# Performance work log

Measured on AMD Instinct MI355X. Metric: run time of the kernel, lower is better.

Reference implementation:

```python
import jax, jax.numpy as jnp
import numpy as np

EPS = 1e-10
B, S, D, K = 8, 2048, 512, 1024
TEMP = 1.0  # quantizer temperature set to 1.0 in SQVAE.__init__


def _ln(x, g, b):
    m = x.mean(-1, keepdims=True)
    v = x.var(-1, keepdims=True)
    return (x - m) / jnp.sqrt(v + 1e-5) * g + b


def _mlp(x, w1, b1, g1, be1, w2, b2, g2, be2):
    # feed_forward: Linear -> ReLU -> LayerNorm, twice (MLPLayers=2)
    h = _ln(jax.nn.relu(x @ w1 + b1), g1, be1)
    return _ln(jax.nn.relu(h @ w2 + b2), g2, be2)


def setup_inputs() -> dict:
    key = jax.random.key(0)
    ks = jax.random.split(key, 20)
    W = 0.04  # small init scale to keep distances / softmax well-conditioned
    p = lambda k, sh, s=1.0: jax.random.normal(k, sh, dtype=jnp.float32) * s
    return {
        'x': p(ks[0], (B, S, D)),
        'gumbel_u': jax.random.uniform(ks[1], (B * S, K), dtype=jnp.float32),
        'enc_w1': p(ks[2], (D, D), W), 'enc_b1': jnp.zeros(D, jnp.float32),
        'enc_g1': jnp.ones(D, jnp.float32), 'enc_be1': jnp.zeros(D, jnp.float32),
        'enc_w2': p(ks[3], (D, D), W), 'enc_b2': jnp.zeros(D, jnp.float32),
        'enc_g2': jnp.ones(D, jnp.float32), 'enc_be2': jnp.zeros(D, jnp.float32),
        'dec_w1': p(ks[4], (D, D), W), 'dec_b1': jnp.zeros(D, jnp.float32),
        'dec_g1': jnp.ones(D, jnp.float32), 'dec_be1': jnp.zeros(D, jnp.float32),
        'dec_w2': p(ks[5], (D, D), W), 'dec_b2': jnp.zeros(D, jnp.float32),
        'dec_g2': jnp.ones(D, jnp.float32), 'dec_be2': jnp.zeros(D, jnp.float32),
        'codebook': p(ks[6], (K, D)),
        'log_param_q': jnp.zeros((), jnp.float32),
    }


def reference(x, gumbel_u, enc_w1, enc_b1, enc_g1, enc_be1, enc_w2, enc_b2, enc_g2, enc_be2,
              dec_w1, dec_b1, dec_g1, dec_be1, dec_w2, dec_b2, dec_g2, dec_be2,
              codebook, log_param_q):
    bs, seq, d = x.shape
    z = _mlp(x, enc_w1, enc_b1, enc_g1, enc_be1, enc_w2, enc_b2, enc_g2, enc_be2)
    # gaussian_1: log_var_q = 0 -> var_q = exp(log_param_q_scalar)
    var_q = jnp.exp(log_param_q)
    w = 0.5 / jnp.clip(var_q, 1e-10)  # 0.5 * precision_q (scalar)
    zf = z.reshape(-1, d)  # [N, D]
    # cdist^2 style distance, scaled by weight -> logits [N, K]
    dist = w * (jnp.sum(zf * zf, axis=1, keepdims=True)
                + jnp.sum(codebook * codebook, axis=1)
                - 2.0 * zf @ codebook.T)
    logit = -dist
    logp = jax.nn.log_softmax(logit, axis=-1)
    probs = jnp.exp(logp)
    # gumbel-softmax sample (train path), noise provided as uniform input
    g = -jnp.log(-jnp.log(gumbel_u + EPS) + EPS)
    encodings = jax.nn.softmax((logit + g) / TEMP, axis=-1)
    z_q = (encodings @ codebook).reshape(bs, seq, d)
    kld_discrete = jnp.sum(probs * logp) / bs
    kld_continuous = jnp.mean(jnp.sum((z - z_q) ** 2 * w, axis=(1, 2)))
    loss = kld_discrete + kld_continuous
    avg_probs = jnp.mean(jax.lax.stop_gradient(probs), axis=0)
    perplexity = jnp.exp(-jnp.sum(avg_probs * jnp.log(avg_probs + 1e-7)))
    x_rec = _mlp(z_q, dec_w1, dec_b1, dec_g1, dec_be1, dec_w2, dec_b2, dec_g2, dec_be2)
    return x_rec, loss, perplexity
```

## Files before the change

### kernel.cpp

```cpp
#include <hip/hip_runtime.h>
#include <math.h>

#define NROWS 16384
#define DIM   512
#define KCODE 1024

typedef __attribute__((ext_vector_type(8))) __bf16 bf16x8;
typedef __attribute__((ext_vector_type(4))) float f32x4;

__device__ __forceinline__ float wave_reduce_sum(float v) {
  #pragma unroll
  for (int m = 1; m < 64; m <<= 1) v += __shfl_xor(v, m, 64);
  return v;
}
__device__ __forceinline__ float wave_reduce_max(float v) {
  #pragma unroll
  for (int m = 1; m < 64; m <<= 1) v = fmaxf(v, __shfl_xor(v, m, 64));
  return v;
}
__device__ __forceinline__ unsigned short f2bf(float f) {
  union { float f; unsigned u; } v; v.f = f;
  unsigned r = v.u + 0x7FFFu + ((v.u >> 16) & 1u);
  return (unsigned short)(r >> 16);
}
__device__ __forceinline__ float bf2f(unsigned short h) {
  union { unsigned u; float f; } v; v.u = ((unsigned)h) << 16;
  return v.f;
}
__device__ __forceinline__ uint4 pack8(const float* x) {
  uint4 r;
  r.x = (unsigned)f2bf(x[0]) | ((unsigned)f2bf(x[1]) << 16);
  r.y = (unsigned)f2bf(x[2]) | ((unsigned)f2bf(x[3]) << 16);
  r.z = (unsigned)f2bf(x[4]) | ((unsigned)f2bf(x[5]) << 16);
  r.w = (unsigned)f2bf(x[6]) | ((unsigned)f2bf(x[7]) << 16);
  return r;
}

__device__ __forceinline__ void glds16(const void* g, void* lds) {
  __builtin_amdgcn_global_load_lds(
      (const __attribute__((address_space(1))) unsigned int*)g,
      (__attribute__((address_space(3))) unsigned int*)lds, 16, 0, 0);
}

template <int NPASS, int EPI, int K, int N, int LDA>
__global__ __launch_bounds__(256) void gemm_bt(
    const unsigned short* A0, const unsigned short* A1, const unsigned short* A2,
    const unsigned short* B0, const unsigned short* B1, const unsigned short* B2,
    const float* __restrict__ bias,
    const float* __restrict__ znorm, const float* __restrict__ cnorm,
    const float* __restrict__ lpq,
    const unsigned short* __restrict__ zh, const unsigned short* __restrict__ zl,
    float* __restrict__ kldc,
    unsigned short* __restrict__ outb, float* __restrict__ outf) {
  __shared__ char smem[32768];
  const int t = threadIdx.x;
  const int l = t & 63, w = t >> 6;
  const int wm = w >> 1, wn = w & 1;
  const int NTN = N / 128;
  const int b = blockIdx.x;
  const int xcd = b & 7;
  const int j = b >> 3;
  const int m0 = (xcd * 16 + j / NTN) * 128;
  const int n0 = (j % NTN) * 128;

  f32x4 acc[4][4];
  #pragma unroll
  for (int i = 0; i < 4; ++i)
    #pragma unroll
    for (int jj = 0; jj < 4; ++jj) acc[i][jj] = (f32x4){0.f, 0.f, 0.f, 0.f};

  const int row_lo = w * 16 + (l & 15);
  const int row_hi = (w + 4) * 16 + (l & 15);
  const int kcol = (l >> 4) * 8;
  const int dA0 = w * 1024;
  const int dA1 = (w + 4) * 1024;
  const int dB0 = 8192 + w * 1024;
  const int dB1 = 8192 + (w + 4) * 1024;

  const unsigned short* APs[3] = {A0, A1, A2};
  const unsigned short* BPs[3] = {B0, B1, B2};

  #pragma unroll 1
  for (int p = 0; p < NPASS; ++p) {
    const unsigned short* aA0 = APs[p] + (size_t)(m0 + row_lo) * LDA + kcol;
    const unsigned short* aA1 = APs[p] + (size_t)(m0 + row_hi) * LDA + kcol;
    const unsigned short* aB0 = BPs[p] + (size_t)(n0 + row_lo) * K + kcol;
    const unsigned short* aB1 = BPs[p] + (size_t)(n0 + row_hi) * K + kcol;
    glds16(aA0, smem + dA0);
    glds16(aA1, smem + dA1);
    glds16(aB0, smem + dB0);
    glds16(aB1, smem + dB1);
    __syncthreads();
    #pragma unroll 1
    for (int kt = 0; kt < K; kt += 32) {
      const int cur = (kt >> 5) & 1;
      const int nxt = cur ^ 1;
      if (kt + 32 < K) {
        char* nb = smem + nxt * 16384;
        glds16(aA0 + kt + 32, nb + dA0);
        glds16(aA1 + kt + 32, nb + dA1);
        glds16(aB0 + kt + 32, nb + dB0);
        glds16(aB1 + kt + 32, nb + dB1);
      }
      const unsigned short* Ab = (const unsigned short*)(smem + cur * 16384);
      const unsigned short* Bb = (const unsigned short*)(smem + cur * 16384 + 8192);
      bf16x8 af[4], bfr[4];
      #pragma unroll
      for (int i = 0; i < 4; ++i) {
        af[i]  = *(const bf16x8*)&Ab[((wm * 4 + i) * 64 + l) * 8];
        bfr[i] = *(const bf16x8*)&Bb[((wn * 4 + i) * 64 + l) * 8];
      }
      #pragma unroll
      for (int mi = 0; mi < 4; ++mi)
        #pragma unroll
        for (int ni = 0; ni < 4; ++ni)
          acc[mi][ni] = __builtin_amdgcn_mfma_f32_16x16x32_bf16(af[mi], bfr[ni], acc[mi][ni], 0, 0, 0);
      __syncthreads();
    }
  }

  float* slab = (float*)(smem + w * 4352);
  const int q = l >> 4, c16 = l & 15;
  const int rr = l >> 4, c4 = (l & 15) * 4;
  const float wq = (EPI >= 1) ? 0.5f / fmaxf(expf(lpq[0]), 1e-10f) : 0.f;
  float local = 0.f;

  #pragma unroll
  for (int mi = 0; mi < 4; ++mi) {
    __syncthreads();
    #pragma unroll
    for (int ni = 0; ni < 4; ++ni)
      #pragma unroll
      for (int r = 0; r < 4; ++r)
        slab[(q * 4 + r) * 68 + ni * 16 + c16] = acc[mi][ni][r];
    __syncthreads();
    #pragma unroll
    for (int pp = 0; pp < 4; ++pp) {
      const int row = pp * 4 + rr;
      const float4 v4 = *(const float4*)&slab[row * 68 + c4];
      float v[4] = {v4.x, v4.y, v4.z, v4.w};
      const int m = m0 + wm * 64 + mi * 16 + row;
      const int nc = n0 + wn * 64 + c4;
      if (EPI == 0) {
        const float4 b4 = *(const float4*)&bias[nc];
        v[0] = fmaxf(v[0] + b4.x, 0.f);
        v[1] = fmaxf(v[1] + b4.y, 0.f);
        v[2] = fmaxf(v[2] + b4.z, 0.f);
        v[3] = fmaxf(v[3] + b4.w, 0.f);
        uint2 st;
        st.x = (unsigned)f2bf(v[0]) | ((unsigned)f2bf(v[1]) << 16);
        st.y = (unsigned)f2bf(v[2]) | ((unsigned)f2bf(v[3]) << 16);
        *(uint2*)&outb[(size_t)m * N + nc] = st;
      } else if (EPI == 1) {
        const float zn = znorm[m];
        const float4 cn = *(const float4*)&cnorm[nc];
        float4 o;
        o.x = -wq * (zn + cn.x - 2.f * v[0]);
        o.y = -wq * (zn + cn.y - 2.f * v[1]);
        o.z = -wq * (zn + cn.z - 2.f * v[2]);
        o.w = -wq * (zn + cn.w - 2.f * v[3]);
        *(float4*)&outf[(size_t)m * N + nc] = o;
      } else {
        const uint2 h2 = *(const uint2*)&zh[(size_t)m * N + nc];
        const uint2 l2 = *(const uint2*)&zl[(size_t)m * N + nc];
        const float z0 = bf2f((unsigned short)(h2.x & 0xFFFF)) + bf2f((unsigned short)(l2.x & 0xFFFF));
        const float z1 = bf2f((unsigned short)(h2.x >> 16))    + bf2f((unsigned short)(l2.x >> 16));
        const float z2 = bf2f((unsigned short)(h2.y & 0xFFFF)) + bf2f((unsigned short)(l2.y & 0xFFFF));
        const float z3 = bf2f((unsigned short)(h2.y >> 16))    + bf2f((unsigned short)(l2.y >> 16));
        const float d0 = z0 - v[0], d1 = z1 - v[1], d2 = z2 - v[2], d3 = z3 - v[3];
        local += d0 * d0 + d1 * d1 + d2 * d2 + d3 * d3;
        uint2 st;
        st.x = (unsigned)f2bf(v[0]) | ((unsigned)f2bf(v[1]) << 16);
        st.y = (unsigned)f2bf(v[2]) | ((unsigned)f2bf(v[3]) << 16);
        *(uint2*)&outb[(size_t)m * N + nc] = st;
      }
    }
  }
  if (EPI == 2) {
    local = wave_reduce_sum(local) * wq;
    if (l == 0) atomicAdd(kldc, local);
  }
}

template <int MODE>
__global__ __launch_bounds__(256) void ln_rows(
    const unsigned short* __restrict__ X, const float* __restrict__ g,
    const float* __restrict__ be, unsigned short* __restrict__ Y,
    unsigned short* __restrict__ Yl, float* __restrict__ znorm,
    float* __restrict__ Yf) {
  const int l = threadIdx.x & 63, wv = threadIdx.x >> 6;
  float gv[8], bv[8];
  {
    const float4 a = *(const float4*)&g[l * 8];
    const float4 b = *(const float4*)&g[l * 8 + 4];
    gv[0] = a.x; gv[1] = a.y; gv[2] = a.z; gv[3] = a.w;
    gv[4] = b.x; gv[5] = b.y; gv[6] = b.z; gv[7] = b.w;
    const float4 c = *(const float4*)&be[l * 8];
    const float4 d = *(const float4*)&be[l * 8 + 4];
    bv[0] = c.x; bv[1] = c.y; bv[2] = c.z; bv[3] = c.w;
    bv[4] = d.x; bv[5] = d.y; bv[6] = d.z; bv[7] = d.w;
  }
  const int row0 = blockIdx.x * 32 + wv * 8;
  for (int rr = 0; rr < 8; ++rr) {
    const int row = row0 + rr;
    const uint4 raw = *(const uint4*)&X[(size_t)row * 512 + l * 8];
    float v[8];
    const unsigned rw[4] = {raw.x, raw.y, raw.z, raw.w};
    #pragma unroll
    for (int i = 0; i < 4; ++i) {
      v[2 * i]     = bf2f((unsigned short)(rw[i] & 0xFFFF));
      v[2 * i + 1] = bf2f((unsigned short)(rw[i] >> 16));
    }
    float s = 0.f, ss = 0.f;
    #pragma unroll
    for (int i = 0; i < 8; ++i) { s += v[i]; ss += v[i] * v[i]; }
    #pragma unroll
    for (int m = 1; m < 64; m <<= 1) {
      s += __shfl_xor(s, m, 64);
      ss += __shfl_xor(ss, m, 64);
    }
    const float mean = s * (1.f / 512.f);
    const float var = ss * (1.f / 512.f) - mean * mean;
    const float rstd = rsqrtf(var + 1e-5f);
    float y[8];
    #pragma unroll
    for (int i = 0; i < 8; ++i) y[i] = (v[i] - mean) * rstd * gv[i] + bv[i];
    if (MODE == 0) {
      *(uint4*)&Y[(size_t)row * 512 + l * 8] = pack8(y);
    } else if (MODE == 1) {
      float lo[8], ns = 0.f;
      unsigned short hx[8];
      #pragma unroll
      for (int i = 0; i < 8; ++i) {
        hx[i] = f2bf(y[i]);
        lo[i] = y[i] - bf2f(hx[i]);
        ns += y[i] * y[i];
      }
      uint4 hv;
      hv.x = (unsigned)hx[0] | ((unsigned)hx[1] << 16);
      hv.y = (unsigned)hx[2] | ((unsigned)hx[3] << 16);
      hv.z = (unsigned)hx[4] | ((unsigned)hx[5] << 16);
      hv.w = (unsigned)hx[6] | ((unsigned)hx[7] << 16);
      *(uint4*)&Y[(size_t)row * 512 + l * 8] = hv;
      *(uint4*)&Yl[(size_t)row * 512 + l * 8] = pack8(lo);
      ns = wave_reduce_sum(ns);
      if (l == 0) znorm[row] = ns;
    } else {
      float4 o0, o1;
      o0.x = y[0]; o0.y = y[1]; o0.z = y[2]; o0.w = y[3];
      o1.x = y[4]; o1.y = y[5]; o1.z = y[6]; o1.w = y[7];
      *(float4*)&Yf[(size_t)row * 512 + l * 8] = o0;
      *(float4*)&Yf[(size_t)row * 512 + l * 8 + 4] = o1;
    }
  }
}

__global__ __launch_bounds__(256) void convert_f32_bf16(
    const float* __restrict__ X, unsigned short* __restrict__ Y) {
  const size_t i = ((size_t)blockIdx.x * 256 + threadIdx.x) * 8;
  const float4 a = *(const float4*)&X[i];
  const float4 b = *(const float4*)&X[i + 4];
  float v[8] = {a.x, a.y, a.z, a.w, b.x, b.y, b.z, b.w};
  *(uint4*)&Y[i] = pack8(v);
}

__global__ __launch_bounds__(256) void prep_cb(
    const float* __restrict__ CB, unsigned short* __restrict__ H,
    unsigned short* __restrict__ L, float* __restrict__ cnorm) {
  const int wv = threadIdx.x >> 6, l = threadIdx.x & 63;
  const int r = blockIdx.x * 4 + wv;
  const float* row = &CB[(size_t)r * 512 + l * 8];
  const float4 a = *(const float4*)row;
  const float4 b = *(const float4*)(row + 4);
  float x[8] = {a.x, a.y, a.z, a.w, b.x, b.y, b.z, b.w};
  float s = 0.f, lo[8];
  unsigned short hi[8];
  #pragma unroll
  for (int i = 0; i < 8; ++i) {
    s += x[i] * x[i];
    hi[i] = f2bf(x[i]);
    lo[i] = x[i] - bf2f(hi[i]);
  }
  uint4 hv;
  hv.x = (unsigned)hi[0] | ((unsigned)hi[1] << 16);
  hv.y = (unsigned)hi[2] | ((unsigned)hi[3] << 16);
  hv.z = (unsigned)hi[4] | ((unsigned)hi[5] << 16);
  hv.w = (unsigned)hi[6] | ((unsigned)hi[7] << 16);
  *(uint4*)&H[(size_t)r * 512 + l * 8] = hv;
  *(uint4*)&L[(size_t)r * 512 + l * 8] = pack8(lo);
  s = wave_reduce_sum(s);
  if (l == 0) cnorm[r] = s;
}

__global__ __launch_bounds__(256) void transpose_f32_bf16(
    const float* __restrict__ in, unsigned short* __restrict__ out, int R, int C) {
  __shared__ float tile[32][33];
  const int ntc = C >> 5;
  const int c0 = (blockIdx.x % ntc) * 32, r0 = (blockIdx.x / ntc) * 32;
  const int tx = threadIdx.x & 31, ty = threadIdx.x >> 5;
  #pragma unroll
  for (int i = 0; i < 4; ++i)
    tile[ty + 8 * i][tx] = in[(size_t)(r0 + ty + 8 * i) * C + c0 + tx];
  __syncthreads();
  #pragma unroll
  for (int i = 0; i < 4; ++i)
    out[(size_t)(c0 + ty + 8 * i) * R + r0 + tx] = f2bf(tile[tx][ty + 8 * i]);
}

__global__ __launch_bounds__(256) void softmax_gumbel(
    const float* logits, const float* __restrict__ U, unsigned short* E,
    float* __restrict__ colsum, float* __restrict__ kldd_acc) {
  __shared__ float cs[1024];
  __shared__ float kd[4];
  const int t = threadIdx.x;
  const int wv = t >> 6, l = t & 63;
  #pragma unroll
  for (int i = 0; i < 4; ++i) cs[t + 256 * i] = 0.f;
  __syncthreads();
  float psum[16];
  #pragma unroll
  for (int i = 0; i < 16; ++i) psum[i] = 0.f;
  float kldd = 0.f;
  const int nbase = blockIdx.x * 16 + wv * 4;

  for (int it = 0; it < 4; ++it) {
    const int row = nbase + it;
    const size_t off = (size_t)row * KCODE + 4 * l;
    float v[16];
    #pragma unroll
    for (int jj = 0; jj < 4; ++jj) {
      const float4 t4 = *(const float4*)&logits[off + 256 * jj];
      v[4 * jj + 0] = t4.x; v[4 * jj + 1] = t4.y; v[4 * jj + 2] = t4.z; v[4 * jj + 3] = t4.w;
    }
    float m = v[0];
    #pragma unroll
    for (int i = 1; i < 16; ++i) m = fmaxf(m, v[i]);
    m = wave_reduce_max(m);
    float se = 0.f;
    #pragma unroll
    for (int i = 0; i < 16; ++i) se += expf(v[i] - m);
    se = wave_reduce_sum(se);
    const float lz = logf(se);
    float pl = 0.f;
    #pragma unroll
    for (int i = 0; i < 16; ++i) {
      const float lp = v[i] - m - lz;
      const float p = expf(lp);
      psum[i] += p;
      pl += p * lp;
    }
    kldd += pl;
    float y[16];
    #pragma unroll
    for (int jj = 0; jj < 4; ++jj) {
      const float4 t4 = *(const float4*)&U[off + 256 * jj];
      y[4 * jj + 0] = v[4 * jj + 0] - logf(-logf(t4.x + 1e-10f) + 1e-10f);
      y[4 * jj + 1] = v[4 * jj + 1] - logf(-logf(t4.y + 1e-10f) + 1e-10f);
      y[4 * jj + 2] = v[4 * jj + 2] - logf(-logf(t4.z + 1e-10f) + 1e-10f);
      y[4 * jj + 3] = v[4 * jj + 3] - logf(-logf(t4.w + 1e-10f) + 1e-10f);
    }
    float m2 = y[0];
    #pragma unroll
    for (int i = 1; i < 16; ++i) m2 = fmaxf(m2, y[i]);
    m2 = wave_reduce_max(m2);
    float s2 = 0.f;
    #pragma unroll
    for (int i = 0; i < 16; ++i) s2 += expf(y[i] - m2);
    s2 = wave_reduce_sum(s2);
    const float inv = 1.f / s2;
    #pragma unroll
    for (int jj = 0; jj < 4; ++jj) {
      ushort4 e;
      e.x = f2bf(expf(y[4 * jj + 0] - m2) * inv);
      e.y = f2bf(expf(y[4 * jj + 1] - m2) * inv);
      e.z = f2bf(expf(y[4 * jj + 2] - m2) * inv);
      e.w = f2bf(expf(y[4 * jj + 3] - m2) * inv);
      *(ushort4*)&E[(size_t)row * 2048 + 4 * l + 256 * jj] = e;
    }
  }
  #pragma unroll
  for (int jj = 0; jj < 4; ++jj)
    #pragma unroll
    for (int c = 0; c < 4; ++c)
      atomicAdd(&cs[256 * jj + 4 * l + c], psum[4 * jj + c]);
  kldd = wave_reduce_sum(kldd);
  if (l == 0) kd[wv] = kldd;
  __syncthreads();
  #pragma unroll
  for (int i = 0; i < 4; ++i) {
    const float vv = cs[t + 256 * i];
    if (vv != 0.f) atomicAdd(&colsum[t + 256 * i], vv);
  }
  if (t == 0) atomicAdd(kldd_acc, kd[0] + kd[1] + kd[2] + kd[3]);
}

__global__ __launch_bounds__(256) void finalize(
    const float* __restrict__ colsum, const float* __restrict__ scal,
    float* __restrict__ out) {
  const int t = threadIdx.x;
  float ent = 0.f;
  #pragma unroll
  for (int jj = 0; jj < 4; ++jj) {
    const float a = colsum[t + 256 * jj] * (1.f / 16384.f);
    ent += a * logf(a + 1e-7f);
  }
  ent = wave_reduce_sum(ent);
  __shared__ float red[4];
  if ((t & 63) == 0) red[t >> 6] = ent;
  __syncthreads();
  if (t == 0) {
    const float tot = red[0] + red[1] + red[2] + red[3];
    out[0] = (scal[0] + scal[1]) * (1.f / 8.f);
    out[1] = expf(-tot);
  }
}

extern "C" void kernel_launch(void* const* d_in, const int* in_sizes, int n_in,
                              void* d_out, int out_size, void* d_ws, size_t ws_size,
                              hipStream_t stream) {
  const float* x      = (const float*)d_in[0];
  const float* gu     = (const float*)d_in[1];
  const float* enc_w1 = (const float*)d_in[2];
  const float* enc_b1 = (const float*)d_in[3];
  const float* enc_g1 = (const float*)d_in[4];
  const float* enc_e1 = (const float*)d_in[5];
  const float* enc_w2 = (const float*)d_in[6];
  const float* enc_b2 = (const float*)d_in[7];
  const float* enc_g2 = (const float*)d_in[8];
  const float* enc_e2 = (const float*)d_in[9];
  const float* dec_w1 = (const float*)d_in[10];
  const float* dec_b1 = (const float*)d_in[11];
  const float* dec_g1 = (const float*)d_in[12];
  const float* dec_e1 = (const float*)d_in[13];
  const float* dec_w2 = (const float*)d_in[14];
  const float* dec_b2 = (const float*)d_in[15];
  const float* dec_g2 = (const float*)d_in[16];
  const float* dec_e2 = (const float*)d_in[17];
  const float* cb     = (const float*)d_in[18];
  const float* lpq    = (const float*)d_in[19];
  float* out = (float*)d_out;
  char* wsb = (char*)d_ws;

  float*          logits = (float*)(wsb + 0);
  unsigned short* Eb     = (unsigned short*)(wsb + 0);
  unsigned short* t1     = (unsigned short*)(wsb + 67108864);
  unsigned short* xb     = (unsigned short*)(wsb + 83886080);
  unsigned short* zh     = xb;
  unsigned short* hq     = (unsigned short*)(wsb + 100663296);
  unsigned short* zl     = (unsigned short*)(wsb + 117440512);
  unsigned short* wt0    = (unsigned short*)(wsb + 134217728);
  unsigned short* wt1    = wt0 + 262144;
  unsigned short* wt2    = wt1 + 262144;
  unsigned short* wt3    = wt2 + 262144;
  unsigned short* cbh    = (unsigned short*)(wsb + 136314880);
  unsigned short* cbl    = (unsigned short*)(wsb + 137363456);
  unsigned short* cbT    = (unsigned short*)(wsb + 138412032);
  float*          znorm  = (float*)(wsb + 139460608);
  float*          cnorm  = (float*)(wsb + 139526144);
  float*          colsum = (float*)(wsb + 139530240);
  float*          scal   = (float*)(wsb + 139534336);

  hipMemsetAsync(colsum, 0, 4096 + 16, stream);

  convert_f32_bf16<<<4096, 256, 0, stream>>>(x, xb);
  prep_cb<<<256, 256, 0, stream>>>(cb, cbh, cbl, cnorm);
  transpose_f32_bf16<<<256, 256, 0, stream>>>(enc_w1, wt0, 512, 512);
  transpose_f32_bf16<<<256, 256, 0, stream>>>(enc_w2, wt1, 512, 512);
  transpose_f32_bf16<<<256, 256, 0, stream>>>(dec_w1, wt2, 512, 512);
  transpose_f32_bf16<<<256, 256, 0, stream>>>(dec_w2, wt3, 512, 512);
  transpose_f32_bf16<<<512, 256, 0, stream>>>(cb, cbT, 1024, 512);

  gemm_bt<1, 0, 512, 512, 512><<<512, 256, 0, stream>>>(
      xb, nullptr, nullptr, wt0, nullptr, nullptr, enc_b1,
      nullptr, nullptr, nullptr, nullptr, nullptr, nullptr, t1, nullptr);
  ln_rows<0><<<512, 256, 0, stream>>>(t1, enc_g1, enc_e1, hq, nullptr, nullptr, nullptr);
  gemm_bt<1, 0, 512, 512, 512><<<512, 256, 0, stream>>>(
      hq, nullptr, nullptr, wt1, nullptr, nullptr, enc_b2,
      nullptr, nullptr, nullptr, nullptr, nullptr, nullptr, t1, nullptr);
  ln_rows<1><<<512, 256, 0, stream>>>(t1, enc_g2, enc_e2, zh, zl, znorm, nullptr);
  gemm_bt<3, 1, 512, 1024, 512><<<1024, 256, 0, stream>>>(
      zh, zl, zh, cbh, cbh, cbl, nullptr,
      znorm, cnorm, lpq, nullptr, nullptr, nullptr, nullptr, logits);
  softmax_gumbel<<<1024, 256, 0, stream>>>(logits, gu, Eb, colsum, &scal[0]);
  gemm_bt<1, 2, 1024, 512, 2048><<<512, 256, 0, stream>>>(
      Eb, nullptr, nullptr, cbT, nullptr, nullptr, nullptr,
      nullptr, nullptr, lpq, zh, zl, &scal[1], hq, nullptr);
  gemm_bt<1, 0, 512, 512, 512><<<512, 256, 0, stream>>>(
      hq, nullptr, nullptr, wt2, nullptr, nullptr, dec_b1,
      nullptr, nullptr, nullptr, nullptr, nullptr, nullptr, t1, nullptr);
  ln_rows<0><<<512, 256, 0, stream>>>(t1, dec_g1, dec_e1, zl, nullptr, nullptr, nullptr);
  gemm_bt<1, 0, 512, 512, 512><<<512, 256, 0, stream>>>(
      zl, nullptr, nullptr, wt3, nullptr, nullptr, dec_b2,
      nullptr, nullptr, nullptr, nullptr, nullptr, nullptr, t1, nullptr);
  ln_rows<2><<<512, 256, 0, stream>>>(t1, dec_g2, dec_e2, nullptr, nullptr, nullptr, out);
  finalize<<<1, 256, 0, stream>>>(colsum, scal, out + 8388608);
}
```

Measured before the change: 529.9 us.

## Add 256x256-tile GEMM for codebook matmuls and flatten multi-pass pipelining

Adds a new 512-thread GEMM kernel with 256x256 output tiles and uses it for the distance-logits and encodings-times-codebook GEMMs. Larger tiles roughly halve the A and B operand traffic per output element. The existing 128-tile GEMM's three split-precision passes are flattened into one software-pipelined step loop. That loop uses explicit vmcnt waits and raw barriers, so the next pass's prefetch no longer stalls at pass boundaries. In exchange it launches far fewer blocks (256 and 128 on a 256-CU part), which may under-fill the device, and it raises register and LDS pressure.

```diff
diff --git a/kernel.cpp b/kernel.cpp
--- a/kernel.cpp
+++ b/kernel.cpp
@@ -40,6 +40,139 @@
   __builtin_amdgcn_global_load_lds(
       (const __attribute__((address_space(1))) unsigned int*)g,
       (__attribute__((address_space(3))) unsigned int*)lds, 16, 0, 0);
+}
+
+template <int NPASS, int EPI, int K, int N, int LDA, int MROWS>
+__global__ __launch_bounds__(512, 2) void gemm256(
+    const unsigned short* A0, const unsigned short* A1, const unsigned short* A2,
+    const unsigned short* B0, const unsigned short* B1, const unsigned short* B2,
+    const float* __restrict__ znorm, const float* __restrict__ cnorm,
+    const float* __restrict__ lpq,
+    const unsigned short* __restrict__ zh, const unsigned short* __restrict__ zl,
+    float* __restrict__ kldc,
+    unsigned short* __restrict__ outb, float* __restrict__ outf) {
+  __shared__ char smem[65536];
+  const int t = threadIdx.x;
+  const int l = t & 63, w = t >> 6;
+  const int wm = w >> 2, wn = w & 3;
+  const int NTN = N / 256;
+  const int b = blockIdx.x;
+  const int xcd = b & 7, j = b >> 3;
+  const int MT_PER_XCD = (MROWS / 256) / 8;
+  const int m0 = (xcd * MT_PER_XCD + j / NTN) * 256;
+  const int n0 = (j % NTN) * 256;
+
+  f32x4 acc[8][4];
+  #pragma unroll
+  for (int i = 0; i < 8; ++i)
+    #pragma unroll
+    for (int jj = 0; jj < 4; ++jj) acc[i][jj] = (f32x4){0.f, 0.f, 0.f, 0.f};
+
+  const int row_lo = w * 16 + (l & 15);
+  const int row_hi = (w + 8) * 16 + (l & 15);
+  const int kcol = (l >> 4) * 8;
+  const int dA0 = w * 1024;
+  const int dA1 = (w + 8) * 1024;
+  const int dB0 = 16384 + w * 1024;
+  const int dB1 = 16384 + (w + 8) * 1024;
+
+  const size_t oA0 = (size_t)(m0 + row_lo) * LDA + kcol;
+  const size_t oA1 = (size_t)(m0 + row_hi) * LDA + kcol;
+  const size_t oB0 = (size_t)(n0 + row_lo) * K + kcol;
+  const size_t oB1 = (size_t)(n0 + row_hi) * K + kcol;
+
+  constexpr int SPP = K / 32;
+  constexpr int NSTEP = NPASS * SPP;
+
+  auto issue = [&](int ss) {
+    const int p = (NPASS == 1) ? 0 : (ss / SPP);
+    const int kt = (ss % SPP) * 32;
+    const unsigned short* A = (p == 0) ? A0 : (p == 1) ? A1 : A2;
+    const unsigned short* B = (p == 0) ? B0 : (p == 1) ? B1 : B2;
+    char* hb = smem + (ss & 1) * 32768;
+    glds16(A + oA0 + kt, hb + dA0);
+    glds16(A + oA1 + kt, hb + dA1);
+    glds16(B + oB0 + kt, hb + dB0);
+    glds16(B + oB1 + kt, hb + dB1);
+  };
+
+  issue(0);
+  #pragma unroll 1
+  for (int s = 0; s < NSTEP; ++s) {
+    if (s + 1 < NSTEP) {
+      issue(s + 1);
+      asm volatile("s_waitcnt vmcnt(4)" ::: "memory");
+    } else {
+      asm volatile("s_waitcnt vmcnt(0)" ::: "memory");
+    }
+    __builtin_amdgcn_s_barrier();
+    const char* hb = smem + (s & 1) * 32768;
+    bf16x8 af[8], bfr[4];
+    #pragma unroll
+    for (int i = 0; i < 4; ++i)
+      bfr[i] = *(const bf16x8*)(hb + 16384 + (wn * 4 + i) * 1024 + l * 16);
+    #pragma unroll
+    for (int i = 0; i < 8; ++i)
+      af[i] = *(const bf16x8*)(hb + (wm * 8 + i) * 1024 + l * 16);
+    #pragma unroll
+    for (int mi = 0; mi < 8; ++mi)
+      #pragma unroll
+      for (int ni = 0; ni < 4; ++ni)
+        acc[mi][ni] = __builtin_amdgcn_mfma_f32_16x16x32_bf16(af[mi], bfr[ni], acc[mi][ni], 0, 0, 0);
+    __builtin_amdgcn_s_barrier();
+  }
+
+  float* slab = (float*)(smem + w * 4352);
+  const int q = l >> 4, c16 = l & 15;
+  const int c4 = (l & 15) * 4;
+  const float wq = 0.5f / fmaxf(expf(lpq[0]), 1e-10f);
+  float local = 0.f;
+
+  #pragma unroll
+  for (int mi = 0; mi < 8; ++mi) {
+    __syncthreads();
+    #pragma unroll
+    for (int ni = 0; ni < 4; ++ni)
+      #pragma unroll
+      for (int r = 0; r < 4; ++r)
+        slab[(q * 4 + r) * 68 + ni * 16 + c16] = acc[mi][ni][r];
+    __syncthreads();
+    #pragma unroll
+    for (int pp = 0; pp < 4; ++pp) {
+      const int row = pp * 4 + q;
+      const float4 v4 = *(const float4*)&slab[row * 68 + c4];
+      float v[4] = {v4.x, v4.y, v4.z, v4.w};
+      const int m = m0 + wm * 128 + mi * 16 + row;
+      const int nc = n0 + wn * 64 + c4;
+      if (EPI == 1) {
+        const float zn = znorm[m];
+        const float4 cn = *(const float4*)&cnorm[nc];
+        float4 o;
+        o.x = -wq * (zn + cn.x - 2.f * v[0]);
+        o.y = -wq * (zn + cn.y - 2.f * v[1]);
+        o.z = -wq * (zn + cn.z - 2.f * v[2]);
+        o.w = -wq * (zn + cn.w - 2.f * v[3]);
+        *(float4*)&outf[(size_t)m * N + nc] = o;
+      } else {
+        const uint2 h2 = *(const uint2*)&zh[(size_t)m * N + nc];
+        const uint2 l2 = *(const uint2*)&zl[(size_t)m * N + nc];
+        const float z0 = bf2f((unsigned short)(h2.x & 0xFFFF)) + bf2f((unsigned short)(l2.x & 0xFFFF));
+        const float z1 = bf2f((unsigned short)(h2.x >> 16))    + bf2f((unsigned short)(l2.x >> 16));
+        const float z2 = bf2f((unsigned short)(h2.y & 0xFFFF)) + bf2f((unsigned short)(l2.y & 0xFFFF));
+        const float z3 = bf2f((unsigned short)(h2.y >> 16))    + bf2f((unsigned short)(l2.y >> 16));
+        const float d0 = z0 - v[0], d1 = z1 - v[1], d2 = z2 - v[2], d3 = z3 - v[3];
+        local += d0 * d0 + d1 * d1 + d2 * d2 + d3 * d3;
+        uint2 st;
+        st.x = (unsigned)f2bf(v[0]) | ((unsigned)f2bf(v[1]) << 16);
+        st.y = (unsigned)f2bf(v[2]) | ((unsigned)f2bf(v[3]) << 16);
+        *(uint2*)&outb[(size_t)m * N + nc] = st;
+      }
+    }
+  }
+  if (EPI == 2) {
+    local = wave_reduce_sum(local) * wq;
+    if (l == 0) atomicAdd(kldc, local);
+  }
 }
 
 template <int NPASS, int EPI, int K, int N, int LDA>
@@ -77,51 +210,54 @@
   const int dB0 = 8192 + w * 1024;
   const int dB1 = 8192 + (w + 4) * 1024;
 
-  const unsigned short* APs[3] = {A0, A1, A2};
-  const unsigned short* BPs[3] = {B0, B1, B2};
-
+  const size_t oA0 = (size_t)(m0 + row_lo) * LDA + kcol;
+  const size_t oA1 = (size_t)(m0 + row_hi) * LDA + kcol;
+  const size_t oB0 = (size_t)(n0 + row_lo) * K + kcol;
+  const size_t oB1 = (size_t)(n0 + row_hi) * K + kcol;
+
+  constexpr int SPP = K / 32;
+  constexpr int NSTEP = NPASS * SPP;
+
+  auto issue = [&](int ss) {
+    const int p = (NPASS == 1) ? 0 : (ss / SPP);
+    const int kt = (ss % SPP) * 32;
+    const unsigned short* A = (p == 0) ? A0 : (p == 1) ? A1 : A2;
+    const unsigned short* B = (p == 0) ? B0 : (p == 1) ? B1 : B2;
+    char* hb = smem + (ss & 1) * 16384;
+    glds16(A + oA0 + kt, hb + dA0);
+    glds16(A + oA1 + kt, hb + dA1);
+    glds16(B + oB0 + kt, hb + dB0);
+    glds16(B + oB1 + kt, hb + dB1);
+  };
+
+  issue(0);
   #pragma unroll 1
-  for (int p = 0; p < NPASS; ++p) {
-    const unsigned short* aA0 = APs[p] + (size_t)(m0 + row_lo) * LDA + kcol;
-    const unsigned short* aA1 = APs[p] + (size_t)(m0 + row_hi) * LDA + kcol;
-    const unsigned short* aB0 = BPs[p] + (size_t)(n0 + row_lo) * K + kcol;
-    const unsigned short* aB1 = BPs[p] + (size_t)(n0 + row_hi) * K + kcol;
-    glds16(aA0, smem + dA0);
-    glds16(aA1, smem + dA1);
-    glds16(aB0, smem + dB0);
-    glds16(aB1, smem + dB1);
-    __syncthreads();
-    #pragma unroll 1
-    for (int kt = 0; kt < K; kt += 32) {
-      const int cur = (kt >> 5) & 1;
-      const int nxt = cur ^ 1;
-      if (kt + 32 < K) {
-        char* nb = smem + nxt * 16384;
-        glds16(aA0 + kt + 32, nb + dA0);
-        glds16(aA1 + kt + 32, nb + dA1);
-        glds16(aB0 + kt + 32, nb + dB0);
-        glds16(aB1 + kt + 32, nb + dB1);
-      }
-      const unsigned short* Ab = (const unsigned short*)(smem + cur * 16384);
-      const unsigned short* Bb = (const unsigned short*)(smem + cur * 16384 + 8192);
-      bf16x8 af[4], bfr[4];
+  for (int s = 0; s < NSTEP; ++s) {
+    if (s + 1 < NSTEP) {
+      issue(s + 1);
+      asm volatile("s_waitcnt vmcnt(4)" ::: "memory");
+    } else {
+      asm volatile("s_waitcnt vmcnt(0)" ::: "memory");
+    }
+    __builtin_amdgcn_s_barrier();
+    const char* hb = smem + (s & 1) * 16384;
+    bf16x8 af[4], bfr[4];
+    #pragma unroll
+    for (int i = 0; i < 4; ++i) {
+      af[i]  = *(const bf16x8*)(hb + (wm * 4 + i) * 1024 + l * 16);
+      bfr[i] = *(const bf16x8*)(hb + 8192 + (wn * 4 + i) * 1024 + l * 16);
+    }
+    #pragma unroll
+    for (int mi = 0; mi < 4; ++mi)
       #pragma unroll
-      for (int i = 0; i < 4; ++i) {
-        af[i]  = *(const bf16x8*)&Ab[((wm * 4 + i) * 64 + l) * 8];
-        bfr[i] = *(const bf16x8*)&Bb[((wn * 4 + i) * 64 + l) * 8];
-      }
-      #pragma unroll
-      for (int mi = 0; mi < 4; ++mi)
-        #pragma unroll
-        for (int ni = 0; ni < 4; ++ni)
-          acc[mi][ni] = __builtin_amdgcn_mfma_f32_16x16x32_bf16(af[mi], bfr[ni], acc[mi][ni], 0, 0, 0);
-      __syncthreads();
-    }
+      for (int ni = 0; ni < 4; ++ni)
+        acc[mi][ni] = __builtin_amdgcn_mfma_f32_16x16x32_bf16(af[mi], bfr[ni], acc[mi][ni], 0, 0, 0);
+    __builtin_amdgcn_s_barrier();
   }
 
   float* slab = (float*)(smem + w * 4352);
   const int q = l >> 4, c16 = l & 15;
-  const int rr = l >> 4, c4 = (l & 15) * 4;
+  const int c4 = (l & 15) * 4;
   const float wq = (EPI >= 1) ? 0.5f / fmaxf(expf(lpq[0]), 1e-10f) : 0.f;
   float local = 0.f;
 
@@ -136,7 +272,7 @@
     __syncthreads();
     #pragma unroll
     for (int pp = 0; pp < 4; ++pp) {
-      const int row = pp * 4 + rr;
+      const int row = pp * 4 + q;
       const float4 v4 = *(const float4*)&slab[row * 68 + c4];
       float v[4] = {v4.x, v4.y, v4.z, v4.w};
       const int m = m0 + wm * 64 + mi * 16 + row;
@@ -478,12 +614,12 @@
       hq, nullptr, nullptr, wt1, nullptr, nullptr, enc_b2,
       nullptr, nullptr, nullptr, nullptr, nullptr, nullptr, t1, nullptr);
   ln_rows<1><<<512, 256, 0, stream>>>(t1, enc_g2, enc_e2, zh, zl, znorm, nullptr);
-  gemm_bt<3, 1, 512, 1024, 512><<<1024, 256, 0, stream>>>(
-      zh, zl, zh, cbh, cbh, cbl, nullptr,
+  gemm256<3, 1, 512, 1024, 512, 16384><<<256, 512, 0, stream>>>(
+      zh, zl, zh, cbh, cbh, cbl,
       znorm, cnorm, lpq, nullptr, nullptr, nullptr, nullptr, logits);
   softmax_gumbel<<<1024, 256, 0, stream>>>(logits, gu, Eb, colsum, &scal[0]);
-  gemm_bt<1, 2, 1024, 512, 2048><<<512, 256, 0, stream>>>(
-      Eb, nullptr, nullptr, cbT, nullptr, nullptr, nullptr,
+  gemm256<1, 2, 1024, 512, 2048, 16384><<<128, 512, 0, stream>>>(
+      Eb, nullptr, nullptr, cbT, nullptr, nullptr,
       nullptr, nullptr, lpq, zh, zl, &scal[1], hq, nullptr);
   gemm_bt<1, 0, 512, 512, 512><<<512, 256, 0, stream>>>(
       hq, nullptr, nullptr, wt2, nullptr, nullptr, dec_b1,
```

Result: no change. 523.1 us (-1.3%).
